# Kernel tuning notes

Hardware: AMD Instinct MI355X
Metric: run time of the kernel (lower is better)

The kernel has to match this reference:

```python
import jax, jax.numpy as jnp
import numpy as np

N = 50000      # nodes
E = 800000     # edges (avg degree 16)
IN = 512       # input_dim
R = 128        # feat_reduce_dim
F = 64         # hid_dim per head
H = 4          # n_heads
OUT = 64       # output_dim
ALPHA = 0.2    # leaky_relu slope


def setup_inputs() -> dict:
    key = jax.random.key(0)
    ks = jax.random.split(key, 12)
    x = jax.random.normal(ks[0], (N, IN), dtype=jnp.float32)
    edges = jax.random.randint(ks[1], (2, E), 0, N, dtype=jnp.int32)
    # per-head GAT layer params (fan-in scaled so exp(logits) stays finite)
    W_lin_h = jax.random.normal(ks[2], (H, R, IN), dtype=jnp.float32) * (IN ** -0.5)
    W_seq_h = jax.random.normal(ks[3], (H, F, R), dtype=jnp.float32) * (R ** -0.5)
    a1_h = jax.random.normal(ks[4], (H, F), dtype=jnp.float32) * (F ** -0.5)
    b1_h = jnp.zeros((H,), dtype=jnp.float32)
    a2_h = jax.random.normal(ks[5], (H, F), dtype=jnp.float32) * (F ** -0.5)
    b2_h = jnp.zeros((H,), dtype=jnp.float32)
    bias_h = jnp.zeros((H, F), dtype=jnp.float32)
    # classifier GAT layer (in = H*F = 256, out = OUT)
    W_lin_c = jax.random.normal(ks[6], (R, H * F), dtype=jnp.float32) * ((H * F) ** -0.5)
    W_seq_c = jax.random.normal(ks[7], (OUT, R), dtype=jnp.float32) * (R ** -0.5)
    a1_c = jax.random.normal(ks[8], (OUT,), dtype=jnp.float32) * (OUT ** -0.5)
    b1_c = jnp.zeros((), dtype=jnp.float32)
    a2_c = jax.random.normal(ks[9], (OUT,), dtype=jnp.float32) * (OUT ** -0.5)
    b2_c = jnp.zeros((), dtype=jnp.float32)
    bias_c = jnp.zeros((OUT,), dtype=jnp.float32)
    return dict(x=x, edges=edges, W_lin_h=W_lin_h, W_seq_h=W_seq_h, a1_h=a1_h,
                b1_h=b1_h, a2_h=a2_h, b2_h=b2_h, bias_h=bias_h,
                W_lin_c=W_lin_c, W_seq_c=W_seq_c, a1_c=a1_c, b1_c=b1_c,
                a2_c=a2_c, b2_c=b2_c, bias_c=bias_c)


def _gat_layer(x, src, dst, W_lin, W_seq, a1, b1, a2, b2, bias, concat):
    n = x.shape[0]
    h = x @ W_lin.T                    # [N, R]   (Linear, no bias)
    s = h @ W_seq.T                    # [N, F]   (Conv1d k=1 == matmul)
    f1 = s @ a1 + b1                   # [N]      (f_1 conv)
    f2 = s @ a2 + b2                   # [N]      (f_2 conv)
    logits = f1[src] + f2[dst]         # [E]  edge-gather
    coefs = jnp.exp(jax.nn.leaky_relu(logits, ALPHA))          # [E]
    denom = jax.ops.segment_sum(coefs, src, num_segments=n)    # [N]
    agg = jax.ops.segment_sum(coefs[:, None] * s[dst], src, num_segments=n)  # [N, F]
    ret = agg / denom[:, None] + bias
    return jax.nn.elu(ret) if concat else ret


def reference(x, edges, W_lin_h, W_seq_h, a1_h, b1_h, a2_h, b2_h, bias_h,
              W_lin_c, W_seq_c, a1_c, b1_c, a2_c, b2_c, bias_c):
    src, dst = edges[0], edges[1]
    # n_heads attention layers (concat=True), vmapped over the head axis
    heads = jax.vmap(
        lambda Wl, Ws, a1, b1, a2, b2, b: _gat_layer(
            x, src, dst, Wl, Ws, a1, b1, a2, b2, b, True)
    )(W_lin_h, W_seq_h, a1_h, b1_h, a2_h, b2_h, bias_h)        # [H, N, F]
    hcat = jnp.transpose(heads, (1, 0, 2)).reshape(x.shape[0], -1)  # [N, H*F]
    # classifier GAT layer (concat=False -> no ELU)
    out = _gat_layer(hcat, src, dst, W_lin_c, W_seq_c, a1_c, b1_c,
                     a2_c, b2_c, bias_c, False)                # [N, OUT]
    return out
```

## Files before the change

kernel.cpp:

```cpp
#include <hip/hip_runtime.h>
#include <hip/hip_bf16.h>
#include <cstddef>
#include <cstdint>

#define IN_DIM 512
#define R_DIM 128
#define F_DIM 64
#define H_NUM 4
#define OUT_DIM 64
#define HF 256

typedef __attribute__((ext_vector_type(4))) float f32x4;
typedef __attribute__((ext_vector_type(8))) short bf16x8;

typedef const __attribute__((address_space(1))) void gas_void;
typedef __attribute__((address_space(3))) void las_void;

__device__ __forceinline__ float bf2f(ushort u) {
    union { uint i; float f; } v; v.i = ((uint)u) << 16; return v.f;
}
__device__ __forceinline__ ushort f2bf(float f) {
    union { float f; uint i; } v; v.f = f;
    uint r = v.i + 0x7fff + ((v.i >> 16) & 1);
    return (ushort)(r >> 16);
}
__device__ __forceinline__ float u2f(uint u) {
    union { uint i; float f; } v; v.i = u; return v.f;
}

__global__ __launch_bounds__(256) void zero_i32(int* __restrict__ p, int n) {
    int i = blockIdx.x * 256 + threadIdx.x;
    if (i < n) p[i] = 0;
}

__global__ __launch_bounds__(256) void wcomb1_kernel(const float* __restrict__ Wlin,
                                                     const float* __restrict__ Wseq,
                                                     ushort* __restrict__ Wc) {
    int idx = blockIdx.x * 256 + threadIdx.x;
    if (idx >= H_NUM * F_DIM * IN_DIM) return;
    int i  = idx & (IN_DIM - 1);
    int hf = idx >> 9;
    int h  = hf >> 6;
    const float* ws = Wseq + (size_t)hf * R_DIM;
    const float* wl = Wlin + (size_t)h * R_DIM * IN_DIM + i;
    float acc = 0.0f;
#pragma unroll 8
    for (int r = 0; r < R_DIM; ++r) acc += ws[r] * wl[(size_t)r * IN_DIM];
    Wc[idx] = f2bf(acc);
}

__global__ __launch_bounds__(256) void wcomb2_kernel(const float* __restrict__ Wlin,
                                                     const float* __restrict__ Wseq,
                                                     ushort* __restrict__ Wc) {
    int idx = blockIdx.x * 256 + threadIdx.x;
    if (idx >= OUT_DIM * HF) return;
    int j = idx & (HF - 1);
    int o = idx >> 8;
    const float* ws = Wseq + (size_t)o * R_DIM;
    const float* wl = Wlin + j;
    float acc = 0.0f;
#pragma unroll 8
    for (int r = 0; r < R_DIM; ++r) acc += ws[r] * wl[(size_t)r * HF];
    Wc[idx] = f2bf(acc);
}

template<int BN, int K, int FS>
__global__ __launch_bounds__(256) void gemm_f32a(const float* __restrict__ A,
                                                 const ushort* __restrict__ B,
                                                 ushort* __restrict__ C,
                                                 int M, int Ntot,
                                                 const float* __restrict__ a1,
                                                 const float* __restrict__ b1,
                                                 const float* __restrict__ a2,
                                                 const float* __restrict__ b2,
                                                 float* __restrict__ f1o,
                                                 float* __restrict__ f2o) {
    constexpr int NF = BN / 16;
    constexpr int HH = BN / 64;
    __shared__ ushort As[64 * 64];
    __shared__ ushort Bs[BN * 64];
    const int tid = threadIdx.x;
    const int wave = tid >> 6;
    const int lane = tid & 63;
    const int lr = lane & 15;
    const int lg = lane >> 4;
    const int m0 = blockIdx.x * 64;

    int base[2];
#pragma unroll
    for (int ks = 0; ks < 2; ++ks)
        base[ks] = lr * 128 + (((ks * 4 + lg) ^ (lr & 7)) * 16);
    const int abase0 = wave * 2048 + base[0];
    const int abase1 = wave * 2048 + base[1];

    f32x4 acc[NF];
#pragma unroll
    for (int cb = 0; cb < NF; ++cb) acc[cb] = (f32x4)0.0f;

    for (int k0 = 0; k0 < K; k0 += 64) {
#pragma unroll
        for (int r = 0; r < BN / 32; ++r) {
            int off = r * 4096 + tid * 16;
            int row = off >> 7;
            int kch = ((off >> 4) & 7) ^ (row & 7);
            const ushort* g = B + (size_t)row * K + k0 + kch * 8;
            __builtin_amdgcn_global_load_lds((gas_void*)g,
                                             (las_void*)((char*)Bs + off), 16, 0, 0);
        }
#pragma unroll
        for (int r = 0; r < 2; ++r) {
            int off = r * 4096 + tid * 16;
            int row = off >> 7;
            int grow = m0 + row;
            if (grow >= M) grow = M - 1;
            int lchunk = (off >> 4) & 7;
            const float* g = A + (size_t)grow * K + k0 + lchunk * 8;
            float4 v0 = *(const float4*)(g);
            float4 v1 = *(const float4*)(g + 4);
            ushort us[8] = {f2bf(v0.x), f2bf(v0.y), f2bf(v0.z), f2bf(v0.w),
                            f2bf(v1.x), f2bf(v1.y), f2bf(v1.z), f2bf(v1.w)};
            int ldsoff = row * 128 + ((lchunk ^ (row & 7)) * 16);
            *(uint4*)((char*)As + ldsoff) = *(const uint4*)us;
        }
        __syncthreads();
        {
            bf16x8 af0 = *(const bf16x8*)((const char*)As + abase0);
            bf16x8 af1 = *(const bf16x8*)((const char*)As + abase1);
#pragma unroll
            for (int cg = 0; cg < NF / 4; ++cg) {
                bf16x8 bfr[4];
#pragma unroll
                for (int j = 0; j < 4; ++j)
                    bfr[j] = *(const bf16x8*)((const char*)Bs + (cg * 4 + j) * 2048 + base[0]);
#pragma unroll
                for (int j = 0; j < 4; ++j)
                    acc[cg * 4 + j] = __builtin_amdgcn_mfma_f32_16x16x32_bf16(
                        af0, bfr[j], acc[cg * 4 + j], 0, 0, 0);
#pragma unroll
                for (int j = 0; j < 4; ++j)
                    bfr[j] = *(const bf16x8*)((const char*)Bs + (cg * 4 + j) * 2048 + base[1]);
#pragma unroll
                for (int j = 0; j < 4; ++j)
                    acc[cg * 4 + j] = __builtin_amdgcn_mfma_f32_16x16x32_bf16(
                        af1, bfr[j], acc[cg * 4 + j], 0, 0, 0);
            }
        }
        __syncthreads();
    }

    float a1v[NF], a2v[NF];
#pragma unroll
    for (int cb = 0; cb < NF; ++cb) {
        int col = cb * 16 + lr;
        a1v[cb] = a1[col];
        a2v[cb] = a2[col];
    }
    const int rowb = m0 + wave * 16 + lg * 4;
#pragma unroll
    for (int r = 0; r < 4; ++r) {
        int row = rowb + r;
        bool ok = row < M;
#pragma unroll
        for (int hh = 0; hh < HH; ++hh) {
            float p1 = 0.f, p2 = 0.f;
#pragma unroll
            for (int c4 = 0; c4 < 4; ++c4) {
                int cb = hh * 4 + c4;
                float v = acc[cb][r];
                p1 += v * a1v[cb];
                p2 += v * a2v[cb];
                if (ok) C[(size_t)row * Ntot + cb * 16 + lr] = f2bf(v);
            }
#pragma unroll
            for (int m = 1; m < 16; m <<= 1) {
                p1 += __shfl_xor(p1, m, 64);
                p2 += __shfl_xor(p2, m, 64);
            }
            if (lr == 0 && ok) {
                f1o[(size_t)row * FS + hh] = p1 + b1[hh];
                f2o[(size_t)row * FS + hh] = p2 + b2[hh];
            }
        }
    }
}

template<int BN, int K, int FS>
__global__ __launch_bounds__(256) void gemm_bf16(const ushort* __restrict__ A,
                                                 const ushort* __restrict__ B,
                                                 ushort* __restrict__ C,
                                                 int M, int Ntot,
                                                 const float* __restrict__ a1,
                                                 const float* __restrict__ b1,
                                                 const float* __restrict__ a2,
                                                 const float* __restrict__ b2,
                                                 float* __restrict__ f1o,
                                                 float* __restrict__ f2o) {
    constexpr int NF = BN / 16;
    constexpr int HH = BN / 64;
    __shared__ ushort As[64 * 64];
    __shared__ ushort Bs[BN * 64];
    const int tid = threadIdx.x;
    const int wave = tid >> 6;
    const int lane = tid & 63;
    const int lr = lane & 15;
    const int lg = lane >> 4;
    const int m0 = blockIdx.x * 64;

    int base[2];
#pragma unroll
    for (int ks = 0; ks < 2; ++ks)
        base[ks] = lr * 128 + (((ks * 4 + lg) ^ (lr & 7)) * 16);
    const int abase0 = wave * 2048 + base[0];
    const int abase1 = wave * 2048 + base[1];

    f32x4 acc[NF];
#pragma unroll
    for (int cb = 0; cb < NF; ++cb) acc[cb] = (f32x4)0.0f;

    for (int k0 = 0; k0 < K; k0 += 64) {
#pragma unroll
        for (int r = 0; r < 2; ++r) {
            int off = r * 4096 + tid * 16;
            int row = off >> 7;
            int kch = ((off >> 4) & 7) ^ (row & 7);
            const ushort* g = A + (size_t)(m0 + row) * K + k0 + kch * 8;
            __builtin_amdgcn_global_load_lds((gas_void*)g,
                                             (las_void*)((char*)As + off), 16, 0, 0);
        }
#pragma unroll
        for (int r = 0; r < BN / 32; ++r) {
            int off = r * 4096 + tid * 16;
            int row = off >> 7;
            int kch = ((off >> 4) & 7) ^ (row & 7);
            const ushort* g = B + (size_t)row * K + k0 + kch * 8;
            __builtin_amdgcn_global_load_lds((gas_void*)g,
                                             (las_void*)((char*)Bs + off), 16, 0, 0);
        }
        __syncthreads();
        {
            bf16x8 af0 = *(const bf16x8*)((const char*)As + abase0);
            bf16x8 af1 = *(const bf16x8*)((const char*)As + abase1);
#pragma unroll
            for (int cg = 0; cg < NF / 4; ++cg) {
                bf16x8 bfr[4];
#pragma unroll
                for (int j = 0; j < 4; ++j)
                    bfr[j] = *(const bf16x8*)((const char*)Bs + (cg * 4 + j) * 2048 + base[0]);
#pragma unroll
                for (int j = 0; j < 4; ++j)
                    acc[cg * 4 + j] = __builtin_amdgcn_mfma_f32_16x16x32_bf16(
                        af0, bfr[j], acc[cg * 4 + j], 0, 0, 0);
#pragma unroll
                for (int j = 0; j < 4; ++j)
                    bfr[j] = *(const bf16x8*)((const char*)Bs + (cg * 4 + j) * 2048 + base[1]);
#pragma unroll
                for (int j = 0; j < 4; ++j)
                    acc[cg * 4 + j] = __builtin_amdgcn_mfma_f32_16x16x32_bf16(
                        af1, bfr[j], acc[cg * 4 + j], 0, 0, 0);
            }
        }
        __syncthreads();
    }

    float a1v[NF], a2v[NF];
#pragma unroll
    for (int cb = 0; cb < NF; ++cb) {
        int col = cb * 16 + lr;
        a1v[cb] = a1[col];
        a2v[cb] = a2[col];
    }
    const int rowb = m0 + wave * 16 + lg * 4;
#pragma unroll
    for (int r = 0; r < 4; ++r) {
        int row = rowb + r;
        bool ok = row < M;
#pragma unroll
        for (int hh = 0; hh < HH; ++hh) {
            float p1 = 0.f, p2 = 0.f;
#pragma unroll
            for (int c4 = 0; c4 < 4; ++c4) {
                int cb = hh * 4 + c4;
                float v = acc[cb][r];
                p1 += v * a1v[cb];
                p2 += v * a2v[cb];
                if (ok) C[(size_t)row * Ntot + cb * 16 + lr] = f2bf(v);
            }
#pragma unroll
            for (int m = 1; m < 16; m <<= 1) {
                p1 += __shfl_xor(p1, m, 64);
                p2 += __shfl_xor(p2, m, 64);
            }
            if (lr == 0 && ok) {
                f1o[(size_t)row * FS + hh] = p1 + b1[hh];
                f2o[(size_t)row * FS + hh] = p2 + b2[hh];
            }
        }
    }
}

__global__ __launch_bounds__(256) void hist_kernel(const int* __restrict__ src,
                                                   int* __restrict__ counts, int E) {
    int e = blockIdx.x * 256 + threadIdx.x;
    if (e < E) atomicAdd(&counts[src[e]], 1);
}

__global__ __launch_bounds__(256) void scan_blk(const int* __restrict__ counts,
                                                int* __restrict__ lexcl,
                                                int* __restrict__ part, int N) {
    __shared__ int wsum[4];
    int t = threadIdx.x;
    int g = blockIdx.x * 256 + t;
    int lane = t & 63, wid = t >> 6;
    int v = (g < N) ? counts[g] : 0;
    int x = v;
#pragma unroll
    for (int off = 1; off < 64; off <<= 1) {
        int u = __shfl_up(x, off, 64);
        if (lane >= off) x += u;
    }
    if (lane == 63) wsum[wid] = x;
    __syncthreads();
    int woff = 0;
#pragma unroll
    for (int w = 0; w < 3; ++w) if (w < wid) woff += wsum[w];
    int incl = x + woff;
    if (g < N) lexcl[g] = incl - v;
    if (t == 255) part[blockIdx.x] = incl;
}

__global__ __launch_bounds__(256) void scan_part(int* __restrict__ part, int nb) {
    __shared__ int wsum[4];
    int t = threadIdx.x;
    int lane = t & 63, wid = t >> 6;
    int v = (t < nb) ? part[t] : 0;
    int x = v;
#pragma unroll
    for (int off = 1; off < 64; off <<= 1) {
        int u = __shfl_up(x, off, 64);
        if (lane >= off) x += u;
    }
    if (lane == 63) wsum[wid] = x;
    __syncthreads();
    int woff = 0;
#pragma unroll
    for (int w = 0; w < 3; ++w) if (w < wid) woff += wsum[w];
    int incl = x + woff;
    __syncthreads();
    if (t < nb) part[t] = incl - v;
    if (t == 255) part[nb] = incl;
}

__global__ __launch_bounds__(256) void scan_add(const int* __restrict__ lexcl,
                                                const int* __restrict__ part,
                                                int* __restrict__ starts,
                                                int* __restrict__ cursor, int N, int nb) {
    int g = blockIdx.x * 256 + threadIdx.x;
    if (g < N) {
        int s = lexcl[g] + part[blockIdx.x];
        starts[g] = s;
        cursor[g] = s;
    }
    if (g == 0) starts[N] = part[nb];
}

__global__ __launch_bounds__(256) void scatter_kernel(const int* __restrict__ src,
                                                      const int* __restrict__ dst,
                                                      int* __restrict__ cursor,
                                                      int* __restrict__ dsts, int E) {
    int e = blockIdx.x * 256 + threadIdx.x;
    if (e >= E) return;
    int p = atomicAdd(&cursor[src[e]], 1);
    dsts[p] = dst[e];
}

__global__ __launch_bounds__(256) void gather1_kernel(const int* __restrict__ starts,
                                                      const int* __restrict__ dsts,
                                                      const float* __restrict__ f1,
                                                      const float* __restrict__ f2,
                                                      const ushort* __restrict__ S1,
                                                      const float* __restrict__ bias,
                                                      ushort* __restrict__ hcat, int N) {
    int n = (int)((blockIdx.x * blockDim.x + threadIdx.x) >> 6);
    int lane = threadIdx.x & 63;
    if (n >= N) return;
    const int head = lane >> 4;
    const float f1h = f1[(size_t)n * 4 + head];
    int beg = starts[n], end = starts[n + 1];
    float a0 = 0.f, a1 = 0.f, a2 = 0.f, a3 = 0.f, den = 0.f;
    int i = beg;
    for (; i + 8 <= end; i += 8) {
        int d[8];
        {
            int4 da = *(const int4*)(dsts + i);
            int4 db = *(const int4*)(dsts + i + 4);
            d[0] = da.x; d[1] = da.y; d[2] = da.z; d[3] = da.w;
            d[4] = db.x; d[5] = db.y; d[6] = db.z; d[7] = db.w;
        }
        float g[8];
        uint2 r[8];
#pragma unroll
        for (int j = 0; j < 8; ++j) {
            g[j] = f2[(size_t)d[j] * 4 + head];
            r[j] = *(const uint2*)(S1 + (size_t)d[j] * HF + lane * 4);
        }
#pragma unroll
        for (int j = 0; j < 8; ++j) {
            float l = f1h + g[j]; l = l > 0.f ? l : 0.2f * l;
            float c = __expf(l);
            a0 += c * u2f(r[j].x << 16);
            a1 += c * u2f(r[j].x & 0xffff0000u);
            a2 += c * u2f(r[j].y << 16);
            a3 += c * u2f(r[j].y & 0xffff0000u);
            den += c;
        }
    }
    if (i + 4 <= end) {
        int4 da = *(const int4*)(dsts + i);
        int d[4] = {da.x, da.y, da.z, da.w};
        float g[4];
        uint2 r[4];
#pragma unroll
        for (int j = 0; j < 4; ++j) {
            g[j] = f2[(size_t)d[j] * 4 + head];
            r[j] = *(const uint2*)(S1 + (size_t)d[j] * HF + lane * 4);
        }
#pragma unroll
        for (int j = 0; j < 4; ++j) {
            float l = f1h + g[j]; l = l > 0.f ? l : 0.2f * l;
            float c = __expf(l);
            a0 += c * u2f(r[j].x << 16);
            a1 += c * u2f(r[j].x & 0xffff0000u);
            a2 += c * u2f(r[j].y << 16);
            a3 += c * u2f(r[j].y & 0xffff0000u);
            den += c;
        }
        i += 4;
    }
    for (; i < end; ++i) {
        int d = dsts[i];
        float g = f2[(size_t)d * 4 + head];
        uint2 r = *(const uint2*)(S1 + (size_t)d * HF + lane * 4);
        float l = f1h + g; l = l > 0.f ? l : 0.2f * l;
        float c = __expf(l);
        a0 += c * u2f(r.x << 16);  a1 += c * u2f(r.x & 0xffff0000u);
        a2 += c * u2f(r.y << 16);  a3 += c * u2f(r.y & 0xffff0000u);
        den += c;
    }
    float rd = __builtin_amdgcn_rcpf(den);
    float4 b = *(const float4*)(bias + lane * 4);
    float v0 = a0 * rd + b.x;
    float v1 = a1 * rd + b.y;
    float v2 = a2 * rd + b.z;
    float v3 = a3 * rd + b.w;
    v0 = v0 > 0.f ? v0 : __expf(v0) - 1.f;
    v1 = v1 > 0.f ? v1 : __expf(v1) - 1.f;
    v2 = v2 > 0.f ? v2 : __expf(v2) - 1.f;
    v3 = v3 > 0.f ? v3 : __expf(v3) - 1.f;
    ushort4 o;
    o.x = f2bf(v0); o.y = f2bf(v1); o.z = f2bf(v2); o.w = f2bf(v3);
    *(ushort4*)(hcat + (size_t)n * HF + lane * 4) = o;
}

__global__ __launch_bounds__(256) void gather2_kernel(const int* __restrict__ starts,
                                                      const int* __restrict__ dsts,
                                                      const float* __restrict__ f1,
                                                      const float* __restrict__ f2,
                                                      const ushort* __restrict__ S2,
                                                      const float* __restrict__ bias,
                                                      float* __restrict__ out, int N) {
    int n = (int)((blockIdx.x * blockDim.x + threadIdx.x) >> 6);
    int lane = threadIdx.x & 63;
    if (n >= N) return;
    const float f1u = f1[n];
    int beg = starts[n], end = starts[n + 1];
    float acc = 0.f, den = 0.f;
    int i = beg;
    for (; i + 8 <= end; i += 8) {
        int d[8];
        {
            int4 da = *(const int4*)(dsts + i);
            int4 db = *(const int4*)(dsts + i + 4);
            d[0] = da.x; d[1] = da.y; d[2] = da.z; d[3] = da.w;
            d[4] = db.x; d[5] = db.y; d[6] = db.z; d[7] = db.w;
        }
        float g[8];
        ushort r[8];
#pragma unroll
        for (int j = 0; j < 8; ++j) {
            g[j] = f2[d[j]];
            r[j] = S2[(size_t)d[j] * OUT_DIM + lane];
        }
#pragma unroll
        for (int j = 0; j < 8; ++j) {
            float l = f1u + g[j]; l = l > 0.f ? l : 0.2f * l;
            float c = __expf(l);
            acc += c * bf2f(r[j]);
            den += c;
        }
    }
    if (i + 4 <= end) {
        int4 da = *(const int4*)(dsts + i);
        int d[4] = {da.x, da.y, da.z, da.w};
        float g[4];
        ushort r[4];
#pragma unroll
        for (int j = 0; j < 4; ++j) {
            g[j] = f2[d[j]];
            r[j] = S2[(size_t)d[j] * OUT_DIM + lane];
        }
#pragma unroll
        for (int j = 0; j < 4; ++j) {
            float l = f1u + g[j]; l = l > 0.f ? l : 0.2f * l;
            float c = __expf(l);
            acc += c * bf2f(r[j]);
            den += c;
        }
        i += 4;
    }
    for (; i < end; ++i) {
        int d = dsts[i];
        float l = f1u + f2[d]; l = l > 0.f ? l : 0.2f * l;
        float c = __expf(l);
        acc += c * bf2f(S2[(size_t)d * OUT_DIM + lane]);
        den += c;
    }
    out[(size_t)n * OUT_DIM + lane] = acc * __builtin_amdgcn_rcpf(den) + bias[lane];
}

extern "C" void kernel_launch(void* const* d_in, const int* in_sizes, int n_in,
                              void* d_out, int out_size, void* d_ws, size_t ws_size,
                              hipStream_t stream) {
    const float* x      = (const float*)d_in[0];
    const int*   edges  = (const int*)d_in[1];
    const float* Wlin_h = (const float*)d_in[2];
    const float* Wseq_h = (const float*)d_in[3];
    const float* a1_h   = (const float*)d_in[4];
    const float* b1_h   = (const float*)d_in[5];
    const float* a2_h   = (const float*)d_in[6];
    const float* b2_h   = (const float*)d_in[7];
    const float* bias_h = (const float*)d_in[8];
    const float* Wlin_c = (const float*)d_in[9];
    const float* Wseq_c = (const float*)d_in[10];
    const float* a1_c   = (const float*)d_in[11];
    const float* b1_c   = (const float*)d_in[12];
    const float* a2_c   = (const float*)d_in[13];
    const float* b2_c   = (const float*)d_in[14];
    const float* bias_c = (const float*)d_in[15];

    const int N = in_sizes[0] / IN_DIM;
    const int E = in_sizes[1] / 2;
    const int* src = edges;
    const int* dst = edges + E;

    char* ws = (char*)d_ws;
    size_t off = 0;
    ushort* WC1   = (ushort*)(ws + off); off += (size_t)HF * IN_DIM * 2;
    ushort* WC2   = (ushort*)(ws + off); off += (size_t)OUT_DIM * HF * 2;
    ushort* S1    = (ushort*)(ws + off); off += (size_t)N * HF * 2;
    ushort* S2    = S1;
    ushort* HCAT  = (ushort*)(ws + off); off += (size_t)N * HF * 2;
    float*  F1    = (float*)(ws + off);  off += (size_t)N * H_NUM * 4;
    float*  F2    = (float*)(ws + off);  off += (size_t)N * H_NUM * 4;
    float*  F1c   = (float*)(ws + off);  off += (size_t)N * 4;
    float*  F2c   = (float*)(ws + off);  off += (size_t)N * 4;
    int* COUNTS   = (int*)(ws + off);    off += (size_t)N * 4;
    int* STARTS   = (int*)(ws + off);    off += ((size_t)N + 1) * 4;
    int* CURSOR   = (int*)(ws + off);    off += (size_t)N * 4;
    int* DSTS     = (int*)(ws + off);    off += (size_t)E * 4;
    int* LEXCL    = (int*)(ws + off);    off += (size_t)N * 4;
    int* PART     = (int*)(ws + off);    off += 512 * 4;

    float* out = (float*)d_out;

    const int eg = (E + 255) / 256;
    const int NB = (N + 255) / 256;

    hipLaunchKernelGGL(zero_i32, dim3(NB), dim3(256), 0, stream, COUNTS, N);
    hipLaunchKernelGGL(hist_kernel, dim3(eg), dim3(256), 0, stream, src, COUNTS, E);
    hipLaunchKernelGGL(scan_blk, dim3(NB), dim3(256), 0, stream, COUNTS, LEXCL, PART, N);
    hipLaunchKernelGGL(scan_part, dim3(1), dim3(256), 0, stream, PART, NB);
    hipLaunchKernelGGL(scan_add, dim3(NB), dim3(256), 0, stream, LEXCL, PART, STARTS, CURSOR, N, NB);
    hipLaunchKernelGGL(scatter_kernel, dim3(eg), dim3(256), 0, stream, src, dst, CURSOR, DSTS, E);

    hipLaunchKernelGGL(wcomb1_kernel, dim3((HF * IN_DIM + 255) / 256), dim3(256),
                       0, stream, Wlin_h, Wseq_h, WC1);
    hipLaunchKernelGGL(wcomb2_kernel, dim3((OUT_DIM * HF + 255) / 256), dim3(256),
                       0, stream, Wlin_c, Wseq_c, WC2);

    hipLaunchKernelGGL((gemm_f32a<HF, IN_DIM, 4>), dim3((N + 63) / 64, 1), dim3(256),
                       0, stream, x, WC1, S1, N, HF,
                       a1_h, b1_h, a2_h, b2_h, F1, F2);

    hipLaunchKernelGGL(gather1_kernel, dim3((N + 3) / 4), dim3(256), 0, stream,
                       STARTS, DSTS, F1, F2, S1, bias_h, HCAT, N);

    hipLaunchKernelGGL((gemm_bf16<OUT_DIM, HF, 1>), dim3((N + 63) / 64, 1), dim3(256),
                       0, stream, HCAT, WC2, S2, N, OUT_DIM,
                       a1_c, b1_c, a2_c, b2_c, F1c, F2c);

    hipLaunchKernelGGL(gather2_kernel, dim3((N + 3) / 4), dim3(256), 0, stream,
                       STARTS, DSTS, F1c, F2c, S2, bias_c, out, N);
}
```

Baseline: 263.7 us.

## Double-buffer LDS tiles in both GEMM kernels to overlap loads with MFMA

Both GEMM kernels now keep two LDS buffers for the A and B tiles and prefetch the next K-tile while running MFMA on the current one. This leaves one barrier per iteration instead of two. In the fp32-A kernel, A is loaded into registers early and converted to bf16 and written to LDS after compute. The cost is twice the LDS footprint and more registers, which may reduce occupancy.

```diff
diff --git a/kernel.cpp b/kernel.cpp
--- a/kernel.cpp
+++ b/kernel.cpp
@@ -77,8 +77,9 @@
                                                  float* __restrict__ f2o) {
     constexpr int NF = BN / 16;
     constexpr int HH = BN / 64;
-    __shared__ ushort As[64 * 64];
-    __shared__ ushort Bs[BN * 64];
+    constexpr int NT = K / 64;
+    __shared__ ushort As[2][64 * 64];
+    __shared__ ushort Bs[2][BN * 64];
     const int tid = threadIdx.x;
     const int wave = tid >> 6;
     const int lane = tid & 63;
@@ -93,60 +94,107 @@
     const int abase0 = wave * 2048 + base[0];
     const int abase1 = wave * 2048 + base[1];
 
+    int s_grow[2], s_ldsoff[2], s_goff[2];
+#pragma unroll
+    for (int r = 0; r < 2; ++r) {
+        int off = r * 4096 + tid * 16;
+        int row = off >> 7;
+        int lchunk = (off >> 4) & 7;
+        int grow = m0 + row;
+        if (grow >= M) grow = M - 1;
+        s_grow[r] = grow;
+        s_goff[r] = lchunk * 8;
+        s_ldsoff[r] = row * 128 + ((lchunk ^ (row & 7)) * 16);
+    }
+
     f32x4 acc[NF];
 #pragma unroll
     for (int cb = 0; cb < NF; ++cb) acc[cb] = (f32x4)0.0f;
 
-    for (int k0 = 0; k0 < K; k0 += 64) {
-#pragma unroll
-        for (int r = 0; r < BN / 32; ++r) {
-            int off = r * 4096 + tid * 16;
-            int row = off >> 7;
-            int kch = ((off >> 4) & 7) ^ (row & 7);
-            const ushort* g = B + (size_t)row * K + k0 + kch * 8;
-            __builtin_amdgcn_global_load_lds((gas_void*)g,
-                                             (las_void*)((char*)Bs + off), 16, 0, 0);
-        }
-#pragma unroll
-        for (int r = 0; r < 2; ++r) {
-            int off = r * 4096 + tid * 16;
-            int row = off >> 7;
-            int grow = m0 + row;
-            if (grow >= M) grow = M - 1;
-            int lchunk = (off >> 4) & 7;
-            const float* g = A + (size_t)grow * K + k0 + lchunk * 8;
-            float4 v0 = *(const float4*)(g);
-            float4 v1 = *(const float4*)(g + 4);
-            ushort us[8] = {f2bf(v0.x), f2bf(v0.y), f2bf(v0.z), f2bf(v0.w),
-                            f2bf(v1.x), f2bf(v1.y), f2bf(v1.z), f2bf(v1.w)};
-            int ldsoff = row * 128 + ((lchunk ^ (row & 7)) * 16);
-            *(uint4*)((char*)As + ldsoff) = *(const uint4*)us;
-        }
+    float4 ar[2][2];
+
+#define ALOAD(K0)                                                          \
+    {                                                                      \
+        _Pragma("unroll")                                                  \
+        for (int r = 0; r < 2; ++r) {                                      \
+            const float* g = A + (size_t)s_grow[r] * K + (K0) + s_goff[r]; \
+            ar[r][0] = *(const float4*)(g);                                \
+            ar[r][1] = *(const float4*)(g + 4);                            \
+        }                                                                  \
+    }
+
+#define AWRITE(BUF)                                                        \
+    {                                                                      \
+        _Pragma("unroll")                                                  \
+        for (int r = 0; r < 2; ++r) {                                      \
+            ushort us[8] = {f2bf(ar[r][0].x), f2bf(ar[r][0].y),            \
+                            f2bf(ar[r][0].z), f2bf(ar[r][0].w),            \
+                            f2bf(ar[r][1].x), f2bf(ar[r][1].y),            \
+                            f2bf(ar[r][1].z), f2bf(ar[r][1].w)};           \
+            *(uint4*)((char*)As[BUF] + s_ldsoff[r]) = *(const uint4*)us;   \
+        }                                                                  \
+    }
+
+#define BSTAGE(BUF, K0)                                                    \
+    {                                                                      \
+        _Pragma("unroll")                                                  \
+        for (int r = 0; r < BN / 32; ++r) {                                \
+            int off = r * 4096 + tid * 16;                                 \
+            int row = off >> 7;                                            \
+            int kch = ((off >> 4) & 7) ^ (row & 7);                        \
+            const ushort* g = B + (size_t)row * K + (K0) + kch * 8;        \
+            __builtin_amdgcn_global_load_lds((gas_void*)g,                 \
+                (las_void*)((char*)Bs[BUF] + off), 16, 0, 0);              \
+        }                                                                  \
+    }
+
+#define COMPUTE(BUF)                                                       \
+    {                                                                      \
+        bf16x8 af0 = *(const bf16x8*)((const char*)As[BUF] + abase0);      \
+        bf16x8 af1 = *(const bf16x8*)((const char*)As[BUF] + abase1);      \
+        _Pragma("unroll")                                                  \
+        for (int cg = 0; cg < NF / 4; ++cg) {                              \
+            bf16x8 bfr[4];                                                 \
+            _Pragma("unroll")                                              \
+            for (int j = 0; j < 4; ++j)                                    \
+                bfr[j] = *(const bf16x8*)((const char*)Bs[BUF] +           \
+                          (cg * 4 + j) * 2048 + base[0]);                  \
+            _Pragma("unroll")                                              \
+            for (int j = 0; j < 4; ++j)                                    \
+                acc[cg * 4 + j] = __builtin_amdgcn_mfma_f32_16x16x32_bf16( \
+                    af0, bfr[j], acc[cg * 4 + j], 0, 0, 0);                \
+            _Pragma("unroll")                                              \
+            for (int j = 0; j < 4; ++j)                                    \
+                bfr[j] = *(const bf16x8*)((const char*)Bs[BUF] +           \
+                          (cg * 4 + j) * 2048 + base[1]);                  \
+            _Pragma("unroll")                                              \
+            for (int j = 0; j < 4; ++j)                                    \
+                acc[cg * 4 + j] = __builtin_amdgcn_mfma_f32_16x16x32_bf16( \
+                    af1, bfr[j], acc[cg * 4 + j], 0, 0, 0);                \
+        }                                                                  \
+    }
+
+    ALOAD(0);
+    BSTAGE(0, 0);
+    AWRITE(0);
+    __syncthreads();
+
+    int buf = 0;
+#pragma unroll
+    for (int t = 0; t < NT - 1; ++t) {
+        ALOAD((t + 1) * 64);
+        BSTAGE(buf ^ 1, (t + 1) * 64);
+        COMPUTE(buf);
+        AWRITE(buf ^ 1);
         __syncthreads();
-        {
-            bf16x8 af0 = *(const bf16x8*)((const char*)As + abase0);
-            bf16x8 af1 = *(const bf16x8*)((const char*)As + abase1);
-#pragma unroll
-            for (int cg = 0; cg < NF / 4; ++cg) {
-                bf16x8 bfr[4];
-#pragma unroll
-                for (int j = 0; j < 4; ++j)
-                    bfr[j] = *(const bf16x8*)((const char*)Bs + (cg * 4 + j) * 2048 + base[0]);
-#pragma unroll
-                for (int j = 0; j < 4; ++j)
-                    acc[cg * 4 + j] = __builtin_amdgcn_mfma_f32_16x16x32_bf16(
-                        af0, bfr[j], acc[cg * 4 + j], 0, 0, 0);
-#pragma unroll
-                for (int j = 0; j < 4; ++j)
-                    bfr[j] = *(const bf16x8*)((const char*)Bs + (cg * 4 + j) * 2048 + base[1]);
-#pragma unroll
-                for (int j = 0; j < 4; ++j)
-                    acc[cg * 4 + j] = __builtin_amdgcn_mfma_f32_16x16x32_bf16(
-                        af1, bfr[j], acc[cg * 4 + j], 0, 0, 0);
-            }
-        }
-        __syncthreads();
-    }
+        buf ^= 1;
+    }
+    COMPUTE(buf);
+
+#undef ALOAD
+#undef AWRITE
+#undef BSTAGE
+#undef COMPUTE
 
     float a1v[NF], a2v[NF];
 #pragma unroll
@@ -197,8 +245,9 @@
                                                  float* __restrict__ f2o) {
     constexpr int NF = BN / 16;
     constexpr int HH = BN / 64;
-    __shared__ ushort As[64 * 64];
-    __shared__ ushort Bs[BN * 64];
+    constexpr int NT = K / 64;
+    __shared__ ushort As[2][64 * 64];
+    __shared__ ushort Bs[2][BN * 64];
     const int tid = threadIdx.x;
     const int wave = tid >> 6;
     const int lane = tid & 63;
@@ -217,50 +266,68 @@
 #pragma unroll
     for (int cb = 0; cb < NF; ++cb) acc[cb] = (f32x4)0.0f;
 
-    for (int k0 = 0; k0 < K; k0 += 64) {
-#pragma unroll
-        for (int r = 0; r < 2; ++r) {
-            int off = r * 4096 + tid * 16;
-            int row = off >> 7;
-            int kch = ((off >> 4) & 7) ^ (row & 7);
-            const ushort* g = A + (size_t)(m0 + row) * K + k0 + kch * 8;
-            __builtin_amdgcn_global_load_lds((gas_void*)g,
-                                             (las_void*)((char*)As + off), 16, 0, 0);
-        }
-#pragma unroll
-        for (int r = 0; r < BN / 32; ++r) {
-            int off = r * 4096 + tid * 16;
-            int row = off >> 7;
-            int kch = ((off >> 4) & 7) ^ (row & 7);
-            const ushort* g = B + (size_t)row * K + k0 + kch * 8;
-            __builtin_amdgcn_global_load_lds((gas_void*)g,
-                                             (las_void*)((char*)Bs + off), 16, 0, 0);
-        }
+#define STAGE(BUF, K0)                                                     \
+    {                                                                      \
+        _Pragma("unroll")                                                  \
+        for (int r = 0; r < 2; ++r) {                                      \
+            int off = r * 4096 + tid * 16;                                 \
+            int row = off >> 7;                                            \
+            int kch = ((off >> 4) & 7) ^ (row & 7);                        \
+            const ushort* g = A + (size_t)(m0 + row) * K + (K0) + kch * 8; \
+            __builtin_amdgcn_global_load_lds((gas_void*)g,                 \
+                (las_void*)((char*)As[BUF] + off), 16, 0, 0);              \
+        }                                                                  \
+        _Pragma("unroll")                                                  \
+        for (int r = 0; r < BN / 32; ++r) {                                \
+            int off = r * 4096 + tid * 16;                                 \
+            int row = off >> 7;                                            \
+            int kch = ((off >> 4) & 7) ^ (row & 7);                        \
+            const ushort* g = B + (size_t)row * K + (K0) + kch * 8;        \
+            __builtin_amdgcn_global_load_lds((gas_void*)g,                 \
+                (las_void*)((char*)Bs[BUF] + off), 16, 0, 0);              \
+        }                                                                  \
+    }
+
+#define COMPUTE(BUF)                                                       \
+    {                                                                      \
+        bf16x8 af0 = *(const bf16x8*)((const char*)As[BUF] + abase0);      \
+        bf16x8 af1 = *(const bf16x8*)((const char*)As[BUF] + abase1);      \
+        _Pragma("unroll")                                                  \
+        for (int cg = 0; cg < NF / 4; ++cg) {                              \
+            bf16x8 bfr[4];                                                 \
+            _Pragma("unroll")                                              \
+            for (int j = 0; j < 4; ++j)                                    \
+                bfr[j] = *(const bf16x8*)((const char*)Bs[BUF] +           \
+                          (cg * 4 + j) * 2048 + base[0]);                  \
+            _Pragma("unroll")                                              \
+            for (int j = 0; j < 4; ++j)                                    \
+                acc[cg * 4 + j] = __builtin_amdgcn_mfma_f32_16x16x32_bf16( \
+                    af0, bfr[j], acc[cg * 4 + j], 0, 0, 0);                \
+            _Pragma("unroll")                                              \
+            for (int j = 0; j < 4; ++j)                                    \
+                bfr[j] = *(const bf16x8*)((const char*)Bs[BUF] +           \
+                          (cg * 4 + j) * 2048 + base[1]);                  \
+            _Pragma("unroll")                                              \
+            for (int j = 0; j < 4; ++j)                                    \
+                acc[cg * 4 + j] = __builtin_amdgcn_mfma_f32_16x16x32_bf16( \
+                    af1, bfr[j], acc[cg * 4 + j], 0, 0, 0);                \
+        }                                                                  \
+    }
+
+    STAGE(0, 0);
+    __syncthreads();
+    int buf = 0;
+#pragma unroll
+    for (int t = 0; t < NT - 1; ++t) {
+        STAGE(buf ^ 1, (t + 1) * 64);
+        COMPUTE(buf);
         __syncthreads();
-        {
-            bf16x8 af0 = *(const bf16x8*)((const char*)As + abase0);
-            bf16x8 af1 = *(const bf16x8*)((const char*)As + abase1);
-#pragma unroll
-            for (int cg = 0; cg < NF / 4; ++cg) {
-                bf16x8 bfr[4];
-#pragma unroll
-                for (int j = 0; j < 4; ++j)
-                    bfr[j] = *(const bf16x8*)((const char*)Bs + (cg * 4 + j) * 2048 + base[0]);
-#pragma unroll
-                for (int j = 0; j < 4; ++j)
-                    acc[cg * 4 + j] = __builtin_amdgcn_mfma_f32_16x16x32_bf16(
-                        af0, bfr[j], acc[cg * 4 + j], 0, 0, 0);
-#pragma unroll
-                for (int j = 0; j < 4; ++j)
-                    bfr[j] = *(const bf16x8*)((const char*)Bs + (cg * 4 + j) * 2048 + base[1]);
-#pragma unroll
-                for (int j = 0; j < 4; ++j)
-                    acc[cg * 4 + j] = __builtin_amdgcn_mfma_f32_16x16x32_bf16(
-                        af1, bfr[j], acc[cg * 4 + j], 0, 0, 0);
-            }
-        }
-        __syncthreads();
-    }
+        buf ^= 1;
+    }
+    COMPUTE(buf);
+
+#undef STAGE
+#undef COMPUTE
 
     float a1v[NF], a2v[NF];
 #pragma unroll
```

Result: slower. 271.4 us (+2.9%).
